# Kernel optimization log

Hardware: AMD Instinct MI355X
Metric: run time of the kernel (lower is better)

The kernel has to match this reference:

```python
import jax, jax.numpy as jnp
import numpy as np

C, B, F, O, DK = 10, 8192, 256, 64, 5


def setup_inputs() -> dict:
    key = jax.random.key(0)
    ks = jax.random.split(key, 7)
    x = jax.random.normal(ks[0], (B, F), jnp.float32)
    y = jax.random.normal(ks[1], (B, C), jnp.float32)
    # kaiming-uniform-like init scales
    w_key = jax.random.normal(ks[2], (C, 1, 1, DK), jnp.float32) * 0.5
    w_query = jax.random.normal(ks[3], (C, 1, DK), jnp.float32) * 0.5
    w_value = jax.random.normal(ks[4], (C, 1, 1), jnp.float32) * 0.5
    weight = jax.random.normal(ks[5], (C, 1, F, O), jnp.float32) * (1.0 / np.sqrt(F))
    bias = jax.random.normal(ks[6], (C, 1, O), jnp.float32) * 0.1
    return {"x": x, "y": y, "w_key": w_key, "w_query": w_query,
            "w_value": w_value, "weight": weight, "bias": bias}


def reference(x, y, w_key, w_query, w_value, weight, bias):
    # x: [B,F] (first=True -> conceptually [1,B,F]); y: [B,C]
    yt = y.T                                             # [C,B]
    querys = yt[..., None] * w_query                     # [C,B,1]*[C,1,DK] -> [C,B,DK]
    # keys[c,b,f,k] = x[b,f] * w_key[c,k]; attn_scores[c,b,f] = sum_k keys*querys
    #              = x[b,f] * (w_key[c] . querys[c,b])  (rank-1 structure, fused)
    kq = jnp.einsum('ck,cbk->cb', w_key.reshape(w_key.shape[0], -1), querys)  # [C,B]
    # mean over batch dim, then softmax over features
    scores_avg = jnp.einsum('bf,cb->cf', x, kq) / x.shape[0]  # [C,F]
    sm = jax.nn.softmax(scores_avg, axis=-1)                  # [C,F]
    attn = sm / jnp.max(sm, axis=-1, keepdims=True)           # [C,F] max-normalized
    values = x[None, :, :] * w_value                          # [1,B,F]*[C,1,1] -> [C,B,F]
    weighted = values * attn[:, None, :]                      # [C,B,F]
    # (weighted[...,None,:] @ weight).squeeze() + bias -> [C,B,O]
    out = jnp.einsum('cbf,cfo->cbo', weighted, weight[:, 0]) + bias  # bias [C,1,O]
    return out
```

## Files before the change

### kernel.cpp

```cpp
#include <hip/hip_runtime.h>
#include <hip/hip_bf16.h>

#define C_ 10
#define B_ 8192
#define F_ 256
#define O_ 64
#define DK_ 5
#define NBLK1 256
#define NG2   16

typedef __attribute__((ext_vector_type(8))) short short8;
typedef __attribute__((ext_vector_type(4))) float floatx4;

static __device__ __forceinline__ unsigned short f2bf(float f) {
    union { float f; unsigned u; } v; v.f = f;
    unsigned r = v.u + 0x7fffu + ((v.u >> 16) & 1u);
    return (unsigned short)(r >> 16);
}

__global__ __launch_bounds__(256) void k1_reduce(const float* __restrict__ x,
                                                 const float* __restrict__ y,
                                                 float* __restrict__ G_part,
                                                 unsigned short* __restrict__ xb) {
    __shared__ float xl[32 * F_];
    __shared__ float yl[32 * C_];
    const int b0 = blockIdx.x * 32;
    const int t  = threadIdx.x;

    for (int i = t; i < 32 * C_; i += 256) yl[i] = y[b0 * C_ + i];

    const int r  = t >> 6;
    const int f4 = (t & 63) * 4;
#pragma unroll
    for (int j = 0; j < 8; ++j) {
        int row = r + 4 * j;
        float4 v = *(const float4*)(x + (size_t)(b0 + row) * F_ + f4);
        *(float4*)(xl + row * F_ + f4) = v;
        ushort4 s;
        s.x = f2bf(v.x); s.y = f2bf(v.y); s.z = f2bf(v.z); s.w = f2bf(v.w);
        *(ushort4*)(xb + (size_t)(b0 + row) * F_ + f4) = s;
    }
    __syncthreads();

    float acc[C_];
#pragma unroll
    for (int c = 0; c < C_; ++c) acc[c] = 0.f;

#pragma unroll 8
    for (int b = 0; b < 32; ++b) {
        float xv = xl[b * F_ + t];
#pragma unroll
        for (int c = 0; c < C_; ++c) acc[c] = fmaf(yl[b * C_ + c], xv, acc[c]);
    }

    float* gp = G_part + (size_t)blockIdx.x * C_ * F_ + t;
#pragma unroll
    for (int c = 0; c < C_; ++c) gp[c * F_] = acc[c];
}

__global__ __launch_bounds__(256) void k1b_reduce(const float* __restrict__ G_part,
                                                  float* __restrict__ G2) {
    const int c = (int)blockIdx.x >> 4;
    const int g = (int)blockIdx.x & 15;
    const int t = threadIdx.x;
    const float* gp = G_part + (size_t)(g * 16) * C_ * F_ + c * F_ + t;
    float a0 = 0.f, a1 = 0.f, a2 = 0.f, a3 = 0.f;
#pragma unroll
    for (int i = 0; i < 16; i += 4) {
        a0 += gp[(size_t)(i + 0) * C_ * F_];
        a1 += gp[(size_t)(i + 1) * C_ * F_];
        a2 += gp[(size_t)(i + 2) * C_ * F_];
        a3 += gp[(size_t)(i + 3) * C_ * F_];
    }
    G2[(size_t)g * C_ * F_ + c * F_ + t] = (a0 + a1) + (a2 + a3);
}

__global__ __launch_bounds__(256) void k3_fused(const unsigned short* __restrict__ xb,
                                                const float* __restrict__ G2,
                                                const float* __restrict__ w_key,
                                                const float* __restrict__ w_query,
                                                const float* __restrict__ w_value,
                                                const float* __restrict__ weight,
                                                const float* __restrict__ bias,
                                                float* __restrict__ out) {
    __shared__ unsigned short wt[O_ * F_];
    __shared__ float a2[F_];
    __shared__ float wred[4];
    const int c  = blockIdx.y;
    const int b0 = blockIdx.x * 64;
    const int t  = threadIdx.x;
    const int w  = t >> 6;
    const int l  = t & 63;
    const int lr = l & 15;
    const int lg = l >> 4;

    const unsigned short* xrow = xb + (size_t)(b0 + w * 16 + lr) * F_;
    short8 a[8];
#pragma unroll
    for (int k0 = 0; k0 < 8; ++k0) a[k0] = *(const short8*)(xrow + k0 * 32 + lg * 8);

    {
        const float* gp = G2 + c * F_ + t;
        float g0 = 0.f, g1 = 0.f, g2 = 0.f, g3 = 0.f;
#pragma unroll
        for (int i = 0; i < NG2; i += 4) {
            g0 += gp[(size_t)(i + 0) * C_ * F_];
            g1 += gp[(size_t)(i + 1) * C_ * F_];
            g2 += gp[(size_t)(i + 2) * C_ * F_];
            g3 += gp[(size_t)(i + 3) * C_ * F_];
        }
        float g = (g0 + g1) + (g2 + g3);

        float s = 0.f;
#pragma unroll
        for (int k = 0; k < DK_; ++k) s += w_key[c * DK_ + k] * w_query[c * DK_ + k];

        float z = s * g * (1.0f / (float)B_);
        float m = z;
#pragma unroll
        for (int off = 32; off >= 1; off >>= 1) m = fmaxf(m, __shfl_xor(m, off));
        if ((t & 63) == 0) wred[t >> 6] = m;
        __syncthreads();
        float mm = fmaxf(fmaxf(wred[0], wred[1]), fmaxf(wred[2], wred[3]));
        a2[t] = expf(z - mm) * w_value[c];
        __syncthreads();
    }

    {
        const float* wsrc = weight + (size_t)c * F_ * O_;
#pragma unroll
        for (int gi = 0; gi < 8; ++gi) {
            int f0 = gi * 32 + w * 8;
            short8 v8;
#pragma unroll
            for (int e = 0; e < 8; ++e) {
                int f = f0 + e;
                v8[e] = (short)f2bf(wsrc[f * O_ + l] * a2[f]);
            }
            int byte = l * 512 + ((2 * f0) ^ ((l & 7) << 4));
            *(short8*)((char*)wt + byte) = v8;
        }
    }
    __syncthreads();

    floatx4 acc[4];
#pragma unroll
    for (int n = 0; n < 4; ++n) {
        float bo = bias[c * O_ + n * 16 + lr];
        acc[n] = (floatx4){bo, bo, bo, bo};
    }

#pragma unroll
    for (int k0 = 0; k0 < 8; ++k0) {
#pragma unroll
        for (int n = 0; n < 4; ++n) {
            int o = n * 16 + lr;
            int byte = o * 512 + ((k0 * 64 + lg * 16) ^ ((o & 7) << 4));
            short8 bf = *(const short8*)((const char*)wt + byte);
            acc[n] = __builtin_amdgcn_mfma_f32_16x16x32_bf16(a[k0], bf, acc[n], 0, 0, 0);
        }
    }

#pragma unroll
    for (int n = 0; n < 4; ++n) {
        int col = n * 16 + lr;
#pragma unroll
        for (int r = 0; r < 4; ++r) {
            int row = b0 + w * 16 + lg * 4 + r;
            out[((size_t)c * B_ + row) * O_ + col] = acc[n][r];
        }
    }
}

extern "C" void kernel_launch(void* const* d_in, const int* in_sizes, int n_in,
                              void* d_out, int out_size, void* d_ws, size_t ws_size,
                              hipStream_t stream) {
    const float* x       = (const float*)d_in[0];
    const float* y       = (const float*)d_in[1];
    const float* w_key   = (const float*)d_in[2];
    const float* w_query = (const float*)d_in[3];
    const float* w_value = (const float*)d_in[4];
    const float* weight  = (const float*)d_in[5];
    const float* bias    = (const float*)d_in[6];
    float* out = (float*)d_out;

    char* ws = (char*)d_ws;
    unsigned short* xb     = (unsigned short*)ws;
    float*          G_part = (float*)(ws + (size_t)B_ * F_ * 2);
    float*          G2     = G_part + (size_t)NBLK1 * C_ * F_;

    k1_reduce<<<NBLK1, 256, 0, stream>>>(x, y, G_part, xb);
    k1b_reduce<<<C_ * NG2, 256, 0, stream>>>(G_part, G2);
    dim3 g3(B_ / 64, C_);
    k3_fused<<<g3, 256, 0, stream>>>(xb, G2, w_key, w_query, w_value, weight, bias, out);
}
```

Measured before the change: 28.52 us.

## Pre-swizzle bf16 weights in reduce kernel and fold attention scaling into x operand

```diff
diff --git a/kernel.cpp b/kernel.cpp
--- a/kernel.cpp
+++ b/kernel.cpp
@@ -20,8 +20,7 @@
 
 __global__ __launch_bounds__(256) void k1_reduce(const float* __restrict__ x,
                                                  const float* __restrict__ y,
-                                                 float* __restrict__ G_part,
-                                                 unsigned short* __restrict__ xb) {
+                                                 float* __restrict__ G_part) {
     __shared__ float xl[32 * F_];
     __shared__ float yl[32 * C_];
     const int b0 = blockIdx.x * 32;
@@ -36,9 +35,6 @@
         int row = r + 4 * j;
         float4 v = *(const float4*)(x + (size_t)(b0 + row) * F_ + f4);
         *(float4*)(xl + row * F_ + f4) = v;
-        ushort4 s;
-        s.x = f2bf(v.x); s.y = f2bf(v.y); s.z = f2bf(v.z); s.w = f2bf(v.w);
-        *(ushort4*)(xb + (size_t)(b0 + row) * F_ + f4) = s;
     }
     __syncthreads();
 
@@ -59,10 +55,13 @@
 }
 
 __global__ __launch_bounds__(256) void k1b_reduce(const float* __restrict__ G_part,
-                                                  float* __restrict__ G2) {
+                                                  const float* __restrict__ weight,
+                                                  float* __restrict__ G2,
+                                                  unsigned short* __restrict__ WTB) {
     const int c = (int)blockIdx.x >> 4;
     const int g = (int)blockIdx.x & 15;
     const int t = threadIdx.x;
+
     const float* gp = G_part + (size_t)(g * 16) * C_ * F_ + c * F_ + t;
     float a0 = 0.f, a1 = 0.f, a2 = 0.f, a3 = 0.f;
 #pragma unroll
@@ -73,18 +72,30 @@
         a3 += gp[(size_t)(i + 3) * C_ * F_];
     }
     G2[(size_t)g * C_ * F_ + c * F_ + t] = (a0 + a1) + (a2 + a3);
-}
-
-__global__ __launch_bounds__(256) void k3_fused(const unsigned short* __restrict__ xb,
+
+    const int o  = t & 63;
+    const int fq = t >> 6;
+    const int f0 = g * 16 + fq * 4;
+    const float* wsrc = weight + (size_t)c * F_ * O_;
+    ushort4 v;
+    v.x = f2bf(wsrc[(f0 + 0) * O_ + o]);
+    v.y = f2bf(wsrc[(f0 + 1) * O_ + o]);
+    v.z = f2bf(wsrc[(f0 + 2) * O_ + o]);
+    v.w = f2bf(wsrc[(f0 + 3) * O_ + o]);
+    char* wb = (char*)(WTB + (size_t)c * O_ * F_);
+    *(ushort4*)(wb + o * 512 + ((2 * f0) ^ ((o & 7) << 4))) = v;
+}
+
+__global__ __launch_bounds__(256) void k3_fused(const float* __restrict__ x,
                                                 const float* __restrict__ G2,
                                                 const float* __restrict__ w_key,
                                                 const float* __restrict__ w_query,
                                                 const float* __restrict__ w_value,
-                                                const float* __restrict__ weight,
                                                 const float* __restrict__ bias,
+                                                const unsigned short* __restrict__ WTB,
                                                 float* __restrict__ out) {
     __shared__ unsigned short wt[O_ * F_];
-    __shared__ float a2[F_];
+    __shared__ float a2s[F_];
     __shared__ float wred[4];
     const int c  = blockIdx.y;
     const int b0 = blockIdx.x * 64;
@@ -94,10 +105,24 @@
     const int lr = l & 15;
     const int lg = l >> 4;
 
-    const unsigned short* xrow = xb + (size_t)(b0 + w * 16 + lr) * F_;
-    short8 a[8];
-#pragma unroll
-    for (int k0 = 0; k0 < 8; ++k0) a[k0] = *(const short8*)(xrow + k0 * 32 + lg * 8);
+    const float* xr = x + (size_t)(b0 + w * 16 + lr) * F_;
+    float4 araw0[8], araw1[8];
+#pragma unroll
+    for (int k0 = 0; k0 < 8; ++k0) {
+        araw0[k0] = *(const float4*)(xr + k0 * 32 + lg * 8);
+        araw1[k0] = *(const float4*)(xr + k0 * 32 + lg * 8 + 4);
+    }
+    const float bo_r = bias[c * O_ + lr];
+    const float bo1  = bias[c * O_ + 16 + lr];
+    const float bo2  = bias[c * O_ + 32 + lr];
+    const float bo3  = bias[c * O_ + 48 + lr];
+
+    {
+        const short8* src = (const short8*)(WTB + (size_t)c * O_ * F_);
+        short8* dst = (short8*)wt;
+#pragma unroll
+        for (int j = 0; j < 8; ++j) dst[t + 256 * j] = src[t + 256 * j];
+    }
 
     {
         const float* gp = G2 + c * F_ + t;
@@ -122,33 +147,33 @@
         if ((t & 63) == 0) wred[t >> 6] = m;
         __syncthreads();
         float mm = fmaxf(fmaxf(wred[0], wred[1]), fmaxf(wred[2], wred[3]));
-        a2[t] = expf(z - mm) * w_value[c];
-        __syncthreads();
-    }
-
-    {
-        const float* wsrc = weight + (size_t)c * F_ * O_;
-#pragma unroll
-        for (int gi = 0; gi < 8; ++gi) {
-            int f0 = gi * 32 + w * 8;
-            short8 v8;
-#pragma unroll
-            for (int e = 0; e < 8; ++e) {
-                int f = f0 + e;
-                v8[e] = (short)f2bf(wsrc[f * O_ + l] * a2[f]);
-            }
-            int byte = l * 512 + ((2 * f0) ^ ((l & 7) << 4));
-            *(short8*)((char*)wt + byte) = v8;
-        }
+        a2s[t] = expf(z - mm) * w_value[c];
     }
     __syncthreads();
 
+    short8 afr[8];
+#pragma unroll
+    for (int k0 = 0; k0 < 8; ++k0) {
+        const int kk = k0 * 32 + lg * 8;
+        float4 s0 = *(const float4*)(a2s + kk);
+        float4 s1 = *(const float4*)(a2s + kk + 4);
+        short8 fr;
+        fr[0] = (short)f2bf(araw0[k0].x * s0.x);
+        fr[1] = (short)f2bf(araw0[k0].y * s0.y);
+        fr[2] = (short)f2bf(araw0[k0].z * s0.z);
+        fr[3] = (short)f2bf(araw0[k0].w * s0.w);
+        fr[4] = (short)f2bf(araw1[k0].x * s1.x);
+        fr[5] = (short)f2bf(araw1[k0].y * s1.y);
+        fr[6] = (short)f2bf(araw1[k0].z * s1.z);
+        fr[7] = (short)f2bf(araw1[k0].w * s1.w);
+        afr[k0] = fr;
+    }
+
     floatx4 acc[4];
-#pragma unroll
-    for (int n = 0; n < 4; ++n) {
-        float bo = bias[c * O_ + n * 16 + lr];
-        acc[n] = (floatx4){bo, bo, bo, bo};
-    }
+    acc[0] = (floatx4){bo_r, bo_r, bo_r, bo_r};
+    acc[1] = (floatx4){bo1, bo1, bo1, bo1};
+    acc[2] = (floatx4){bo2, bo2, bo2, bo2};
+    acc[3] = (floatx4){bo3, bo3, bo3, bo3};
 
 #pragma unroll
     for (int k0 = 0; k0 < 8; ++k0) {
@@ -157,7 +182,7 @@
             int o = n * 16 + lr;
             int byte = o * 512 + ((k0 * 64 + lg * 16) ^ ((o & 7) << 4));
             short8 bf = *(const short8*)((const char*)wt + byte);
-            acc[n] = __builtin_amdgcn_mfma_f32_16x16x32_bf16(a[k0], bf, acc[n], 0, 0, 0);
+            acc[n] = __builtin_amdgcn_mfma_f32_16x16x32_bf16(afr[k0], bf, acc[n], 0, 0, 0);
         }
     }
 
@@ -185,12 +210,12 @@
     float* out = (float*)d_out;
 
     char* ws = (char*)d_ws;
-    unsigned short* xb     = (unsigned short*)ws;
-    float*          G_part = (float*)(ws + (size_t)B_ * F_ * 2);
+    float*          G_part = (float*)ws;
     float*          G2     = G_part + (size_t)NBLK1 * C_ * F_;
-
-    k1_reduce<<<NBLK1, 256, 0, stream>>>(x, y, G_part, xb);
-    k1b_reduce<<<C_ * NG2, 256, 0, stream>>>(G_part, G2);
+    unsigned short* WTB    = (unsigned short*)(G2 + (size_t)NG2 * C_ * F_);
+
+    k1_reduce<<<NBLK1, 256, 0, stream>>>(x, y, G_part);
+    k1b_reduce<<<C_ * NG2, 256, 0, stream>>>(G_part, weight, G2, WTB);
     dim3 g3(B_ / 64, C_);
-    k3_fused<<<g3, 256, 0, stream>>>(xb, G2, w_key, w_query, w_value, weight, bias, out);
-}
+    k3_fused<<<g3, 256, 0, stream>>>(x, G2, w_key, w_query, w_value, bias, WTB, out);
+}
```

Result: slower. 29.16 us (+2.2%).
